# Kernel tuning notes

Measured on AMD Instinct MI355X. Metric: run time of the kernel, lower is better.

## Reference

```python
import jax, jax.numpy as jnp
import numpy as np

B, N, C, H, P = 4, 8192, 256, 4, 64  # batch, tokens(=input_size), hidden, heads, proj_size
D = C // H


def setup_inputs() -> dict:
    key = jax.random.key(0)
    ks = jax.random.split(key, 12)
    s = 1.0 / np.sqrt(C)
    inp = {
        "x": jax.random.normal(ks[0], (B, N, C), jnp.float32),
        "q": jax.random.normal(ks[1], (B, N, C), jnp.float32),
        "Wq": jax.random.normal(ks[2], (C, C), jnp.float32) * s,
        "Wk": jax.random.normal(ks[3], (C, C), jnp.float32) * s,
        "Wv_ca": jax.random.normal(ks[4], (C, C), jnp.float32) * s,
        "Wv_sa": jax.random.normal(ks[5], (C, C), jnp.float32) * s,
        "E_w": jax.random.normal(ks[6], (P, N), jnp.float32) * (1.0 / np.sqrt(N)),
        "E_b": jnp.zeros((P,), jnp.float32),
        "temp": jnp.ones((H, 1, 1), jnp.float32),
        "temp2": jnp.ones((H, 1, 1), jnp.float32),
        "Wo1": jax.random.normal(ks[7], (C // 2, C), jnp.float32) * s,
        "bo1": jnp.zeros((C // 2,), jnp.float32),
        "Wo2": jax.random.normal(ks[8], (C // 2, C), jnp.float32) * s,
        "bo2": jnp.zeros((C // 2,), jnp.float32),
    }
    return inp


def _l2norm(t):
    # F.normalize(dim=-1): x / max(||x||_2, 1e-12)
    n = jnp.sqrt(jnp.sum(t * t, axis=-1, keepdims=True))
    return t / jnp.maximum(n, 1e-12)


def reference(x, q, Wq, Wk, Wv_ca, Wv_sa, E_w, E_b, temp, temp2, Wo1, bo1, Wo2, bo2):
    b, n, c = x.shape
    h, d = H, c // H

    def split(t):  # [B,N,C] -> [B,H,d,N]
        return t.reshape(b, n, h, d).transpose(0, 2, 3, 1)

    qs = split(q @ Wq.T)
    ks = split(x @ Wk.T)
    v_ca = split(x @ Wv_ca.T)
    v_sa = split(x @ Wv_sa.T)

    # Linformer-style projections E (=F) over token dim N -> P
    k_proj = jnp.einsum('bhdn,pn->bhdp', ks, E_w) + E_b   # [B,H,d,P]
    v_proj = jnp.einsum('bhdn,pn->bhdp', v_sa, E_w) + E_b  # [B,H,d,P]

    qn = _l2norm(qs)
    kn = _l2norm(ks)

    # Channel attention: [B,H,d,d]
    attn_ca = jax.nn.softmax(jnp.einsum('bhdn,bhen->bhde', qn, kn) * temp, axis=-1)
    x_ca = jnp.einsum('bhde,bhen->bhdn', attn_ca, v_ca)
    x_ca = x_ca.transpose(0, 3, 1, 2).reshape(b, n, c)

    # Spatial (projected) attention: [B,H,N,P]
    attn_sa = jax.nn.softmax(jnp.einsum('bhdn,bhdp->bhnp', qn, k_proj) * temp2, axis=-1)
    x_sa = jnp.einsum('bhnp,bhdp->bhnd', attn_sa, v_proj)
    # faithful to original permute(0,3,1,2).reshape(B,N,C)
    x_sa = x_sa.transpose(0, 3, 1, 2).reshape(b, n, c)

    x_sa = x_sa @ Wo1.T + bo1
    x_ca = x_ca @ Wo2.T + bo2
    return jnp.concatenate((x_sa, x_ca), axis=-1)
```

## Files before the change

### kernel.cpp

```cpp
#include <hip/hip_runtime.h>
#include <hip/hip_bf16.h>

#define NN 8192
#define BNC 8388608

typedef unsigned short u16;
typedef unsigned int u32;
typedef __attribute__((ext_vector_type(8))) short bf16x8;
typedef __attribute__((ext_vector_type(4))) float f32x4;
typedef __attribute__((ext_vector_type(4))) float float4v;

__device__ __forceinline__ float bf2f(u16 u) {
    union { u32 i; float f; } c; c.i = ((u32)u) << 16; return c.f;
}
__device__ __forceinline__ u16 f2bf(float f) {
    union { float f; u32 i; } c; c.f = f;
    u32 x = c.i;
    u32 r = (x + 0x7fffu + ((x >> 16) & 1u)) >> 16;
    return (u16)r;
}
__device__ __forceinline__ void gl16(const u16* g, u16* l) {
    __builtin_amdgcn_global_load_lds(
        (const __attribute__((address_space(1))) void*)g,
        (__attribute__((address_space(3))) void*)l, 16, 0, 0);
}

__global__ void fill_kernel(float* __restrict__ out, float val) {
    int base = (blockIdx.x * 256 + threadIdx.x) * 4;
    #pragma unroll
    for (int i = 0; i < 4; ++i) out[base + i] = val;
}

__global__ void zeroconv_kernel(const float* __restrict__ x,
                                const float* __restrict__ Wq, const float* __restrict__ Wk,
                                const float* __restrict__ Wo1, const float* __restrict__ Ew,
                                u16* __restrict__ xb,
                                u16* __restrict__ Wqb, u16* __restrict__ Wkb,
                                u16* __restrict__ Wo1b, u16* __restrict__ Ewb,
                                float* __restrict__ zbase) {
    if (blockIdx.x >= 4432) {
        int i = (blockIdx.x - 4432) * 256 + threadIdx.x;
        if (i < 67584) zbase[i] = 0.f;
        return;
    }
    size_t e = ((size_t)blockIdx.x * 256 + threadIdx.x) * 8;
    const float* src; u16* dst;
    if (e < 8388608)      { src = x   + e;             dst = xb   + e; }
    else if (e < 8454144) { src = Wq  + (e - 8388608); dst = Wqb  + (e - 8388608); }
    else if (e < 8519680) { src = Wk  + (e - 8454144); dst = Wkb  + (e - 8454144); }
    else if (e < 8552448) { src = Wo1 + (e - 8519680); dst = Wo1b + (e - 8519680); }
    else                  { src = Ew  + (e - 8552448); dst = Ewb  + (e - 8552448); }
    float4v f0 = *(const float4v*)src, f1 = *(const float4v*)(src + 4);
    bf16x8 v;
    #pragma unroll
    for (int j = 0; j < 4; ++j) {
        v[j] = (short)f2bf(f0[j]); v[4 + j] = (short)f2bf(f1[j]);
    }
    *(bf16x8*)dst = v;
}

__global__ __launch_bounds__(256) void qkxe_kernel(
    const float* __restrict__ qf, const u16* __restrict__ xb,
    const u16* __restrict__ Wqb, const u16* __restrict__ Wkb,
    u16* __restrict__ Qb, u16* __restrict__ Kb,
    float* __restrict__ nq2, float* __restrict__ nk2,
    const u16* __restrict__ Ewb, float* __restrict__ xE)
{
    __shared__ u16 sm[17408];
    const int t = threadIdx.x, lane = t & 63, w = t >> 6;
    const int fr = lane & 15, fk = (lane >> 4) * 8, r0 = (lane >> 4) * 4;

    if (blockIdx.x < 1024) {
        u16* As = sm;
        u16* Bs = sm + 4096;
        const int mt = blockIdx.x & 255, nt = (blockIdx.x >> 8) & 1, z = blockIdx.x >> 9;
        const u16* Bt = z ? Wkb : Wqb;
        u16* O = z ? Kb : Qb;
        float* dstn = z ? nk2 : nq2;
        const int wr = w >> 1, wc = w & 1;
        const int m0 = mt * 128, n0 = nt * 128;
        const int b = m0 >> 13;
        const int row0 = t >> 2, k80 = (t & 3) * 8;
        const int row1 = (256 + t) >> 2, k81 = ((256 + t) & 3) * 8;

        f32x4 acc[4][4];
        #pragma unroll
        for (int i = 0; i < 4; ++i)
            #pragma unroll
            for (int j = 0; j < 4; ++j) acc[i][j] = (f32x4){0.f, 0.f, 0.f, 0.f};

        for (int kt = 0; kt < 8; ++kt) {
            const int k0 = kt * 32;
            if (z == 0) {
                const float* p0 = qf + (size_t)(m0 + row0) * 256 + k0 + k80;
                float4v f0 = *(const float4v*)p0, f1 = *(const float4v*)(p0 + 4);
                bf16x8 va;
                #pragma unroll
                for (int j = 0; j < 4; ++j) {
                    va[j] = (short)f2bf(f0[j]); va[4 + j] = (short)f2bf(f1[j]);
                }
                *(bf16x8*)&As[t * 8] = va;
                const float* p1 = qf + (size_t)(m0 + row1) * 256 + k0 + k81;
                float4v g0 = *(const float4v*)p1, g1 = *(const float4v*)(p1 + 4);
                bf16x8 vb2;
                #pragma unroll
                for (int j = 0; j < 4; ++j) {
                    vb2[j] = (short)f2bf(g0[j]); vb2[4 + j] = (short)f2bf(g1[j]);
                }
                *(bf16x8*)&As[(256 + t) * 8] = vb2;
            } else {
                gl16(xb + (size_t)(m0 + row0) * 256 + k0 + k80, &As[t * 8]);
                gl16(xb + (size_t)(m0 + row1) * 256 + k0 + k81, &As[(256 + t) * 8]);
            }
            gl16(Bt + (size_t)(n0 + row0) * 256 + k0 + k80, &Bs[t * 8]);
            gl16(Bt + (size_t)(n0 + row1) * 256 + k0 + k81, &Bs[(256 + t) * 8]);
            __syncthreads();
            bf16x8 a[4], bfr[4];
            #pragma unroll
            for (int fm = 0; fm < 4; ++fm)
                a[fm] = *(const bf16x8*)&As[(wr * 64 + fm * 16 + fr) * 32 + fk];
            #pragma unroll
            for (int fn = 0; fn < 4; ++fn)
                bfr[fn] = *(const bf16x8*)&Bs[(wc * 64 + fn * 16 + fr) * 32 + fk];
            #pragma unroll
            for (int fm = 0; fm < 4; ++fm)
                #pragma unroll
                for (int fn = 0; fn < 4; ++fn)
                    acc[fm][fn] = __builtin_amdgcn_mfma_f32_16x16x32_bf16(
                        a[fm], bfr[fn], acc[fm][fn], 0, 0, 0);
            __syncthreads();
        }

        #pragma unroll
        for (int fn = 0; fn < 4; ++fn) {
            int gcol = n0 + wc * 64 + fn * 16 + fr;
            float s = 0.f;
            #pragma unroll
            for (int fm = 0; fm < 4; ++fm) {
                #pragma unroll
                for (int r = 0; r < 4; ++r) {
                    size_t grow = (size_t)(m0 + wr * 64 + fm * 16 + r0 + r);
                    float v = acc[fm][fn][r];
                    O[grow * 256 + gcol] = f2bf(v);
                    s += v * v;
                }
            }
            s += __shfl_xor(s, 16);
            s += __shfl_xor(s, 32);
            if (lane < 16) atomicAdd(&dstn[b * 256 + gcol], s);
        }
    } else {
        u16 (*smA)[136] = (u16(*)[136])sm;
        u16 (*smB)[136] = (u16(*)[136])(sm + 8704);
        const int bx2 = blockIdx.x - 1024;
        const int bkq = bx2 >> 4, nc = bx2 & 15;
        const int b = bkq >> 2, kq = bkq & 3;

        f32x4 acc[4][4];
        #pragma unroll
        for (int i = 0; i < 4; ++i)
            #pragma unroll
            for (int j = 0; j < 4; ++j) acc[i][j] = (f32x4){0.f, 0.f, 0.f, 0.f};

        for (int it = 0; it < 4; ++it) {
            const int n0 = nc * 512 + it * 128;
            #pragma unroll
            for (int i = 0; i < 4; ++i) {
                int c = i * 256 + t, tok = c >> 3, kl = (c & 7) * 8;
                const int sw = tok ^ ((kl >> 3) << 3);
                bf16x8 v = *(const bf16x8*)(xb + ((size_t)b * NN + n0 + tok) * 256 + kq * 64 + kl);
                #pragma unroll
                for (int j = 0; j < 8; ++j) smA[kl + j][sw] = (u16)v[j];
            }
            #pragma unroll
            for (int i = 0; i < 4; ++i) {
                int c = i * 256 + t, p = c >> 4, tk8 = (c & 15) * 8;
                *(bf16x8*)&smB[p][tk8] = *(const bf16x8*)(Ewb + (size_t)p * NN + n0 + tk8);
            }
            __syncthreads();
            bf16x8 a[4], bb[4];
            #pragma unroll
            for (int fm = 0; fm < 4; ++fm) {
                int row = fm * 16 + fr;
                a[fm] = *(const bf16x8*)&smA[row][(w * 32 + fk) ^ (((row >> 3) & 7) << 3)];
            }
            #pragma unroll
            for (int fn = 0; fn < 4; ++fn)
                bb[fn] = *(const bf16x8*)&smB[fn * 16 + fr][w * 32 + fk];
            #pragma unroll
            for (int fm = 0; fm < 4; ++fm)
                #pragma unroll
                for (int fn = 0; fn < 4; ++fn)
                    acc[fm][fn] = __builtin_amdgcn_mfma_f32_16x16x32_bf16(
                        a[fm], bb[fn], acc[fm][fn], 0, 0, 0);
            __syncthreads();
        }
        float* Cred = (float*)&smA[0][0];
        for (int ph = 0; ph < 4; ++ph) {
            if (w == ph) {
                #pragma unroll
                for (int fm = 0; fm < 4; ++fm)
                    #pragma unroll
                    for (int fn = 0; fn < 4; ++fn)
                        #pragma unroll
                        for (int r = 0; r < 4; ++r) {
                            int idx = (fm * 16 + r0 + r) * 64 + fn * 16 + fr;
                            if (ph == 0) Cred[idx] = acc[fm][fn][r];
                            else         Cred[idx] += acc[fm][fn][r];
                        }
            }
            __syncthreads();
        }
        float* dst = xE + (size_t)(b * 256 + kq * 64) * 64;
        #pragma unroll
        for (int i = 0; i < 16; ++i) atomicAdd(&dst[i * 256 + t], Cred[i * 256 + t]);
    }
}

__global__ __launch_bounds__(256) void calogkv_kernel(
    const u16* __restrict__ Qb, const u16* __restrict__ Kb, float* __restrict__ cpart,
    const float* __restrict__ Wk, const float* __restrict__ Wvsa,
    const float* __restrict__ xE, const float* __restrict__ Eb,
    float* __restrict__ kp, float* __restrict__ vp)
{
    __shared__ u16 sm[17408];
    const int t = threadIdx.x, lane = t & 63, w = t >> 6;
    const int fr = lane & 15, fk = (lane >> 4) * 8, r0 = (lane >> 4) * 4;

    if (blockIdx.x < 256) {
        u16 (*smA)[136] = (u16(*)[136])sm;
        u16 (*smB)[136] = (u16(*)[136])(sm + 8704);
        const int bh = blockIdx.x >> 4, nc = blockIdx.x & 15;
        const int b = bh >> 2, h = bh & 3;

        f32x4 acc[4][4];
        #pragma unroll
        for (int i = 0; i < 4; ++i)
            #pragma unroll
            for (int j = 0; j < 4; ++j) acc[i][j] = (f32x4){0.f, 0.f, 0.f, 0.f};

        for (int it = 0; it < 4; ++it) {
            const int n0 = nc * 512 + it * 128;
            #pragma unroll
            for (int i = 0; i < 4; ++i) {
                int c = i * 256 + t, tok = c >> 3, ch8 = (c & 7) * 8;
                const int sw = tok ^ ((ch8 >> 3) << 3);
                size_t g = ((size_t)b * NN + n0 + tok) * 256 + h * 64 + ch8;
                bf16x8 vq = *(const bf16x8*)(Qb + g);
                bf16x8 vk = *(const bf16x8*)(Kb + g);
                #pragma unroll
                for (int j = 0; j < 8; ++j) {
                    smA[ch8 + j][sw] = (u16)vq[j];
                    smB[ch8 + j][sw] = (u16)vk[j];
                }
            }
            __syncthreads();
            bf16x8 a[4], bb[4];
            #pragma unroll
            for (int fm = 0; fm < 4; ++fm) {
                int row = fm * 16 + fr;
                a[fm] = *(const bf16x8*)&smA[row][(w * 32 + fk) ^ (((row >> 3) & 7) << 3)];
            }
            #pragma unroll
            for (int fn = 0; fn < 4; ++fn) {
                int row = fn * 16 + fr;
                bb[fn] = *(const bf16x8*)&smB[row][(w * 32 + fk) ^ (((row >> 3) & 7) << 3)];
            }
            #pragma unroll
            for (int fm = 0; fm < 4; ++fm)
                #pragma unroll
                for (int fn = 0; fn < 4; ++fn)
                    acc[fm][fn] = __builtin_amdgcn_mfma_f32_16x16x32_bf16(
                        a[fm], bb[fn], acc[fm][fn], 0, 0, 0);
            __syncthreads();
        }
        float* Cred = (float*)&smA[0][0];
        for (int ph = 0; ph < 4; ++ph) {
            if (w == ph) {
                #pragma unroll
                for (int fm = 0; fm < 4; ++fm)
                    #pragma unroll
                    for (int fn = 0; fn < 4; ++fn)
                        #pragma unroll
                        for (int r = 0; r < 4; ++r) {
                            int idx = (fm * 16 + r0 + r) * 64 + fn * 16 + fr;
                            if (ph == 0) Cred[idx] = acc[fm][fn][r];
                            else         Cred[idx] += acc[fm][fn][r];
                        }
            }
            __syncthreads();
        }
        float* dst = cpart + (size_t)nc * 65536 + (size_t)bh * 4096;
        #pragma unroll
        for (int i = 0; i < 16; ++i) dst[i * 256 + t] = Cred[i * 256 + t];
    } else {
        const int idx = blockIdx.x - 256;
        const int z = idx >> 8, bc4 = idx & 255;
        const int b = bc4 >> 6, c = (bc4 & 63) * 4 + (t >> 6);
        const int p = t & 63;
        const float* W = z ? Wvsa : Wk;
        float* dst = z ? vp : kp;
        float s = 0.f;
        for (int k = 0; k < 256; ++k)
            s += W[c * 256 + k] * xE[(size_t)(b * 256 + k) * 64 + p];
        dst[(size_t)(b * 256 + c) * 64 + p] = s + Eb[p];
    }
}

__global__ __launch_bounds__(256) void smsa_kernel(
    const float* __restrict__ cpart, const float* __restrict__ nq2,
    const float* __restrict__ nk2, const float* __restrict__ temp,
    float* __restrict__ caprob,
    const u16* __restrict__ Qb, const float* __restrict__ kp,
    const float* __restrict__ vp, const float* __restrict__ temp2,
    u16* __restrict__ xsa)
{
    __shared__ char smem[49152];
    const int t = threadIdx.x;
    if (blockIdx.x < 256) {
        const int row = blockIdx.x * 4 + (t >> 6);
        const int e = t & 63;
        const int b = row >> 8, c = row & 255, h = c >> 6;
        const int i = row * 64 + e;
        float lg = cpart[i];
        #pragma unroll
        for (int nc = 1; nc < 16; ++nc) lg += cpart[(size_t)nc * 65536 + i];
        float nq = fmaxf(sqrtf(nq2[row]), 1e-12f);
        float nk = fmaxf(sqrtf(nk2[b * 256 + h * 64 + e]), 1e-12f);
        float v = lg / (nq * nk) * temp[h];
        float m = v;
        #pragma unroll
        for (int o = 32; o; o >>= 1) m = fmaxf(m, __shfl_xor(m, o));
        float ex = __expf(v - m);
        float s = ex;
        #pragma unroll
        for (int o = 32; o; o >>= 1) s += __shfl_xor(s, o);
        caprob[i] = ex / s;
        return;
    }
    u16* Qs = (u16*)smem;
    u16* KT = (u16*)(smem + 32768);
    u16* VT = (u16*)(smem + 40960);
    const int bx2 = blockIdx.x - 256;
    const int nc = bx2 & 31, bh = bx2 >> 5, b = bh >> 2, h = bh & 3;
    const int lane = t & 63, w = t >> 6;
    const int fr = lane & 15, fk = (lane >> 4) * 8, r0 = (lane >> 4) * 4;

    #pragma unroll
    for (int i = 0; i < 8; ++i) {
        int c = i * 256 + t, tok = c >> 3, ch8 = (c & 7) * 8;
        *(bf16x8*)&Qs[c * 8] =
            *(const bf16x8*)(Qb + ((size_t)b * NN + nc * 256 + tok) * 256 + h * 64 + ch8);
    }
    {
        const int d = t >> 2, p0 = (t & 3) * 16;
        const float rqv = 1.0f / fmaxf(sqrtf(nq2[b * 256 + h * 64 + d]), 1e-12f);
        const float t2 = temp2[h];
        const float* kr = kp + (size_t)(b * 256 + h * 64 + d) * 64 + p0;
        #pragma unroll
        for (int j = 0; j < 16; ++j)
            KT[(p0 + j) * 64 + d] = f2bf(kr[j] * rqv * t2);
    }
    {
        const float* vs = vp + (size_t)(b * 256 + h * 64) * 64;
        #pragma unroll
        for (int i = 0; i < 2; ++i) {
            int c = i * 256 + t;
            bf16x8 v;
            #pragma unroll
            for (int j = 0; j < 8; ++j) v[j] = (short)f2bf(vs[c * 8 + j]);
            *(bf16x8*)&VT[c * 8] = v;
        }
    }
    __syncthreads();

    f32x4 acc[4][4];
    #pragma unroll
    for (int i = 0; i < 4; ++i)
        #pragma unroll
        for (int j = 0; j < 4; ++j) acc[i][j] = (f32x4){0.f, 0.f, 0.f, 0.f};
    #pragma unroll
    for (int ks = 0; ks < 2; ++ks) {
        bf16x8 a[4], bb[4];
        #pragma unroll
        for (int fm = 0; fm < 4; ++fm)
            a[fm] = *(const bf16x8*)&Qs[(w * 64 + fm * 16 + fr) * 64 + ks * 32 + fk];
        #pragma unroll
        for (int fn = 0; fn < 4; ++fn)
            bb[fn] = *(const bf16x8*)&KT[(fn * 16 + fr) * 64 + ks * 32 + fk];
        #pragma unroll
        for (int fm = 0; fm < 4; ++fm)
            #pragma unroll
            for (int fn = 0; fn < 4; ++fn)
                acc[fm][fn] = __builtin_amdgcn_mfma_f32_16x16x32_bf16(
                    a[fm], bb[fn], acc[fm][fn], 0, 0, 0);
    }
    __syncthreads();

    u16* Pw = Qs + w * 4096;
    #pragma unroll
    for (int fm = 0; fm < 4; ++fm) {
        #pragma unroll
        for (int r = 0; r < 4; ++r) {
            float m = fmaxf(fmaxf(acc[fm][0][r], acc[fm][1][r]),
                            fmaxf(acc[fm][2][r], acc[fm][3][r]));
            m = fmaxf(m, __shfl_xor(m, 1));
            m = fmaxf(m, __shfl_xor(m, 2));
            m = fmaxf(m, __shfl_xor(m, 4));
            m = fmaxf(m, __shfl_xor(m, 8));
            float e0 = __expf(acc[fm][0][r] - m), e1 = __expf(acc[fm][1][r] - m);
            float e2 = __expf(acc[fm][2][r] - m), e3 = __expf(acc[fm][3][r] - m);
            float s = e0 + e1 + e2 + e3;
            s += __shfl_xor(s, 1); s += __shfl_xor(s, 2);
            s += __shfl_xor(s, 4); s += __shfl_xor(s, 8);
            float rs = 1.0f / s;
            int row = fm * 16 + r0 + r;
            Pw[row * 64 +  0 + fr] = f2bf(e0 * rs);
            Pw[row * 64 + 16 + fr] = f2bf(e1 * rs);
            Pw[row * 64 + 32 + fr] = f2bf(e2 * rs);
            Pw[row * 64 + 48 + fr] = f2bf(e3 * rs);
        }
    }

    f32x4 acc2[4][4];
    #pragma unroll
    for (int i = 0; i < 4; ++i)
        #pragma unroll
        for (int j = 0; j < 4; ++j) acc2[i][j] = (f32x4){0.f, 0.f, 0.f, 0.f};
    #pragma unroll
    for (int ks = 0; ks < 2; ++ks) {
        bf16x8 a[4], bb[4];
        #pragma unroll
        for (int fm = 0; fm < 4; ++fm)
            a[fm] = *(const bf16x8*)&Pw[(fm * 16 + fr) * 64 + ks * 32 + fk];
        #pragma unroll
        for (int fn = 0; fn < 4; ++fn)
            bb[fn] = *(const bf16x8*)&VT[(fn * 16 + fr) * 64 + ks * 32 + fk];
        #pragma unroll
        for (int fm = 0; fm < 4; ++fm)
            #pragma unroll
            for (int fn = 0; fn < 4; ++fn)
                acc2[fm][fn] = __builtin_amdgcn_mfma_f32_16x16x32_bf16(
                    a[fm], bb[fn], acc2[fm][fn], 0, 0, 0);
    }
    __syncthreads();

    u16* X2 = Qs;
    #pragma unroll
    for (int fm = 0; fm < 4; ++fm)
        #pragma unroll
        for (int fn = 0; fn < 4; ++fn)
            #pragma unroll
            for (int r = 0; r < 4; ++r)
                X2[(w * 64 + fm * 16 + r0 + r) * 64 + fn * 16 + fr] = f2bf(acc2[fm][fn][r]);
    __syncthreads();

    {
        const int d = t >> 2, cq = (t & 3) * 64;
        u16* orow = xsa + ((size_t)b * NN + d * 128 + h * 32 + nc) * 256 + cq;
        #pragma unroll
        for (int i = 0; i < 8; ++i) {
            bf16x8 v;
            #pragma unroll
            for (int j = 0; j < 8; ++j) v[j] = (short)X2[(cq + i * 8 + j) * 64 + d];
            *(bf16x8*)&orow[i * 8] = v;
        }
    }
}

__device__ __forceinline__ void out_gemm_body(
    const u16* __restrict__ A, const u16* __restrict__ Bt,
    const float* __restrict__ bias, int outoff, int m0,
    float* __restrict__ out, u16* As, u16* Bs, int t)
{
    const int lane = t & 63, w = t >> 6;
    const int wr = w >> 1, wc = w & 1;
    const int fr = lane & 15, fk = (lane >> 4) * 8, r0 = (lane >> 4) * 4;
    const int row0 = t >> 2, k80 = (t & 3) * 8;
    const int row1 = (256 + t) >> 2, k81 = ((256 + t) & 3) * 8;

    f32x4 acc[4][4];
    #pragma unroll
    for (int i = 0; i < 4; ++i)
        #pragma unroll
        for (int j = 0; j < 4; ++j) acc[i][j] = (f32x4){0.f, 0.f, 0.f, 0.f};

    for (int kt = 0; kt < 8; ++kt) {
        const int k0 = kt * 32;
        gl16(A  + (size_t)(m0 + row0) * 256 + k0 + k80, &As[t * 8]);
        gl16(A  + (size_t)(m0 + row1) * 256 + k0 + k81, &As[(256 + t) * 8]);
        gl16(Bt + (size_t)row0 * 256 + k0 + k80, &Bs[t * 8]);
        gl16(Bt + (size_t)row1 * 256 + k0 + k81, &Bs[(256 + t) * 8]);
        __syncthreads();
        bf16x8 a[4], bfr[4];
        #pragma unroll
        for (int fm = 0; fm < 4; ++fm)
            a[fm] = *(const bf16x8*)&As[(wr * 64 + fm * 16 + fr) * 32 + fk];
        #pragma unroll
        for (int fn = 0; fn < 4; ++fn)
            bfr[fn] = *(const bf16x8*)&Bs[(wc * 64 + fn * 16 + fr) * 32 + fk];
        #pragma unroll
        for (int fm = 0; fm < 4; ++fm)
            #pragma unroll
            for (int fn = 0; fn < 4; ++fn)
                acc[fm][fn] = __builtin_amdgcn_mfma_f32_16x16x32_bf16(
                    a[fm], bfr[fn], acc[fm][fn], 0, 0, 0);
        __syncthreads();
    }

    #pragma unroll
    for (int fm = 0; fm < 4; ++fm)
        #pragma unroll
        for (int fn = 0; fn < 4; ++fn) {
            int gcol = wc * 64 + fn * 16 + fr;
            #pragma unroll
            for (int r = 0; r < 4; ++r) {
                size_t grow = (size_t)(m0 + wr * 64 + fm * 16 + r0 + r);
                out[grow * 256 + outoff + gcol] = acc[fm][fn][r] + bias[gcol];
            }
        }
}

__global__ __launch_bounds__(256) void mwout_kernel(
    const float* __restrict__ caprob, const float* __restrict__ Wo2,
    const float* __restrict__ Wvca, u16* __restrict__ W2effb,
    const u16* __restrict__ xsa, const u16* __restrict__ Wo1b,
    const float* __restrict__ bo1, float* __restrict__ out)
{
    __shared__ u16 sm[8192];
    const int t = threadIdx.x;
    if (blockIdx.x < 512) {
        float* Ml = (float*)sm;
        const int bj = blockIdx.x;
        const int b = bj >> 7, j = bj & 127;
        const int h = t >> 6, e = t & 63;
        float s = 0.f;
        #pragma unroll 8
        for (int d = 0; d < 64; ++d)
            s += Wo2[j * 256 + h * 64 + d] * caprob[(size_t)(b * 256 + h * 64 + d) * 64 + e];
        Ml[t] = s;
        __syncthreads();
        float s2 = 0.f;
        for (int c = 0; c < 256; ++c) s2 += Ml[c] * Wvca[c * 256 + t];
        W2effb[(size_t)bj * 256 + t] = f2bf(s2);
        return;
    }
    const int m0 = (blockIdx.x - 512) * 128;
    out_gemm_body(xsa, Wo1b, bo1, 0, m0, out, sm, sm + 4096, t);
}

__global__ __launch_bounds__(256) void outca_kernel(
    const u16* __restrict__ xb, const u16* __restrict__ W2effb,
    const float* __restrict__ bo2, float* __restrict__ out)
{
    __shared__ u16 sm[8192];
    const int t = threadIdx.x;
    const int m0 = blockIdx.x * 128;
    const u16* Bt = W2effb + (size_t)(blockIdx.x >> 6) * 128 * 256;
    out_gemm_body(xb, Bt, bo2, 128, m0, out, sm, sm + 4096, t);
}

extern "C" void kernel_launch(void* const* d_in, const int* in_sizes, int n_in,
                              void* d_out, int out_size, void* d_ws, size_t ws_size,
                              hipStream_t stream) {
    float* out = (float*)d_out;

    static const int expect[14] = {8388608, 8388608, 65536, 65536, 65536, 65536,
                                   524288, 64, 4, 4, 32768, 128, 32768, 128};
    bool ok = (n_in == 14) && (out_size == 8388608);
    if (ok) for (int i = 0; i < 14; ++i) ok = ok && (in_sizes[i] == expect[i]);
    if (!ok) {
        fill_kernel<<<dim3(8192), 256, 0, stream>>>(out, 3000.0f);
        return;
    }
    if (ws_size < 80000000u) {
        fill_kernel<<<dim3(8192), 256, 0, stream>>>(out, 1000.0f);
        return;
    }

    const float* x    = (const float*)d_in[0];
    const float* q    = (const float*)d_in[1];
    const float* Wq   = (const float*)d_in[2];
    const float* Wk   = (const float*)d_in[3];
    const float* Wvca = (const float*)d_in[4];
    const float* Wvsa = (const float*)d_in[5];
    const float* Ew   = (const float*)d_in[6];
    const float* Eb   = (const float*)d_in[7];
    const float* temp = (const float*)d_in[8];
    const float* temp2= (const float*)d_in[9];
    const float* Wo1  = (const float*)d_in[10];
    const float* bo1  = (const float*)d_in[11];
    const float* Wo2  = (const float*)d_in[12];
    const float* bo2  = (const float*)d_in[13];

    u16* Qb   = (u16*)d_ws;
    u16* Kb   = Qb + (size_t)BNC;
    u16* xb   = Kb + (size_t)BNC;
    u16* Wqb  = xb + (size_t)BNC;
    u16* Wkb  = Wqb + 65536;
    u16* Wo1b = Wkb + 65536;
    u16* Ewb  = Wo1b + 32768;
    u16* W2effb = Ewb + 524288;
    u16* xsa  = Kb;
    float* fs    = (float*)(W2effb + 131072);
    float* nq2   = fs;
    float* nk2   = nq2 + 1024;
    float* xE    = nk2 + 1024;
    float* kp    = xE + 65536;
    float* vp    = kp + 65536;
    float* caprob= vp + 65536;
    float* cpart = caprob + 65536;

    zeroconv_kernel<<<dim3(4696), 256, 0, stream>>>(x, Wq, Wk, Wo1, Ew,
                                                    xb, Wqb, Wkb, Wo1b, Ewb, nq2);
    qkxe_kernel<<<dim3(1280), 256, 0, stream>>>(q, xb, Wqb, Wkb, Qb, Kb, nq2, nk2,
                                                Ewb, xE);
    calogkv_kernel<<<dim3(768), 256, 0, stream>>>(Qb, Kb, cpart, Wk, Wvsa, xE, Eb, kp, vp);
    smsa_kernel<<<dim3(768), 256, 0, stream>>>(cpart, nq2, nk2, temp, caprob,
                                               Qb, kp, vp, temp2, xsa);
    mwout_kernel<<<dim3(768), 256, 0, stream>>>(caprob, Wo2, Wvca, W2effb,
                                                xsa, Wo1b, bo1, out);
    outca_kernel<<<dim3(256), 256, 0, stream>>>(xb, W2effb, bo2, out);
}
```

Before: 105.5 us.

## Use 128-wide K tiles with XOR-swizzled LDS layout in Q/K projection GEMM

The Q/K projection GEMM now stages 128-wide K chunks into LDS, so each block runs two iterations instead of eight, with four MFMA sub-steps per iteration. An XOR swizzle on the column index, applied both when loading and when reading fragments, is meant to avoid LDS bank conflicts. This cuts barrier count and load-phase overhead. In exchange, LDS use per block grows from 34 KB to 64 KB, which may reduce occupancy, and the other branches of the same kernel also carry this larger allocation.

```diff
diff --git a/kernel.cpp b/kernel.cpp
--- a/kernel.cpp
+++ b/kernel.cpp
@@ -66,13 +66,13 @@
     float* __restrict__ nq2, float* __restrict__ nk2,
     const u16* __restrict__ Ewb, float* __restrict__ xE)
 {
-    __shared__ u16 sm[17408];
+    __shared__ u16 sm[32768];
     const int t = threadIdx.x, lane = t & 63, w = t >> 6;
     const int fr = lane & 15, fk = (lane >> 4) * 8, r0 = (lane >> 4) * 4;
 
     if (blockIdx.x < 1024) {
         u16* As = sm;
-        u16* Bs = sm + 4096;
+        u16* Bs = sm + 16384;
         const int mt = blockIdx.x & 255, nt = (blockIdx.x >> 8) & 1, z = blockIdx.x >> 9;
         const u16* Bt = z ? Wkb : Wqb;
         u16* O = z ? Kb : Qb;
@@ -80,8 +80,6 @@
         const int wr = w >> 1, wc = w & 1;
         const int m0 = mt * 128, n0 = nt * 128;
         const int b = m0 >> 13;
-        const int row0 = t >> 2, k80 = (t & 3) * 8;
-        const int row1 = (256 + t) >> 2, k81 = ((256 + t) & 3) * 8;
 
         f32x4 acc[4][4];
         #pragma unroll
@@ -89,45 +87,49 @@
             #pragma unroll
             for (int j = 0; j < 4; ++j) acc[i][j] = (f32x4){0.f, 0.f, 0.f, 0.f};
 
-        for (int kt = 0; kt < 8; ++kt) {
-            const int k0 = kt * 32;
-            if (z == 0) {
-                const float* p0 = qf + (size_t)(m0 + row0) * 256 + k0 + k80;
-                float4v f0 = *(const float4v*)p0, f1 = *(const float4v*)(p0 + 4);
-                bf16x8 va;
-                #pragma unroll
-                for (int j = 0; j < 4; ++j) {
-                    va[j] = (short)f2bf(f0[j]); va[4 + j] = (short)f2bf(f1[j]);
+        for (int kt = 0; kt < 2; ++kt) {
+            const int k0 = kt * 128;
+            #pragma unroll
+            for (int i = 0; i < 8; ++i) {
+                int c = i * 256 + t, row = c >> 4, kc8 = (c & 15) * 8;
+                int ksrc = kc8 ^ ((row & 7) << 3);
+                if (z == 0) {
+                    const float* p = qf + (size_t)(m0 + row) * 256 + k0 + ksrc;
+                    float4v f0 = *(const float4v*)p, f1 = *(const float4v*)(p + 4);
+                    bf16x8 va;
+                    #pragma unroll
+                    for (int j = 0; j < 4; ++j) {
+                        va[j] = (short)f2bf(f0[j]); va[4 + j] = (short)f2bf(f1[j]);
+                    }
+                    *(bf16x8*)&As[c * 8] = va;
+                } else {
+                    gl16(xb + (size_t)(m0 + row) * 256 + k0 + ksrc, &As[c * 8]);
                 }
-                *(bf16x8*)&As[t * 8] = va;
-                const float* p1 = qf + (size_t)(m0 + row1) * 256 + k0 + k81;
-                float4v g0 = *(const float4v*)p1, g1 = *(const float4v*)(p1 + 4);
-                bf16x8 vb2;
-                #pragma unroll
-                for (int j = 0; j < 4; ++j) {
-                    vb2[j] = (short)f2bf(g0[j]); vb2[4 + j] = (short)f2bf(g1[j]);
+                gl16(Bt + (size_t)(n0 + row) * 256 + k0 + ksrc, &Bs[c * 8]);
+            }
+            __syncthreads();
+            #pragma unroll
+            for (int ks = 0; ks < 4; ++ks) {
+                bf16x8 a[4], bfr[4];
+                #pragma unroll
+                for (int fm = 0; fm < 4; ++fm) {
+                    int row = wr * 64 + fm * 16 + fr;
+                    a[fm] = *(const bf16x8*)&As[row * 128 +
+                             ((ks * 32 + fk) ^ ((row & 7) << 3))];
                 }
-                *(bf16x8*)&As[(256 + t) * 8] = vb2;
-            } else {
-                gl16(xb + (size_t)(m0 + row0) * 256 + k0 + k80, &As[t * 8]);
-                gl16(xb + (size_t)(m0 + row1) * 256 + k0 + k81, &As[(256 + t) * 8]);
-            }
-            gl16(Bt + (size_t)(n0 + row0) * 256 + k0 + k80, &Bs[t * 8]);
-            gl16(Bt + (size_t)(n0 + row1) * 256 + k0 + k81, &Bs[(256 + t) * 8]);
-            __syncthreads();
-            bf16x8 a[4], bfr[4];
-            #pragma unroll
-            for (int fm = 0; fm < 4; ++fm)
-                a[fm] = *(const bf16x8*)&As[(wr * 64 + fm * 16 + fr) * 32 + fk];
-            #pragma unroll
-            for (int fn = 0; fn < 4; ++fn)
-                bfr[fn] = *(const bf16x8*)&Bs[(wc * 64 + fn * 16 + fr) * 32 + fk];
-            #pragma unroll
-            for (int fm = 0; fm < 4; ++fm)
-                #pragma unroll
-                for (int fn = 0; fn < 4; ++fn)
-                    acc[fm][fn] = __builtin_amdgcn_mfma_f32_16x16x32_bf16(
-                        a[fm], bfr[fn], acc[fm][fn], 0, 0, 0);
+                #pragma unroll
+                for (int fn = 0; fn < 4; ++fn) {
+                    int row = wc * 64 + fn * 16 + fr;
+                    bfr[fn] = *(const bf16x8*)&Bs[row * 128 +
+                              ((ks * 32 + fk) ^ ((row & 7) << 3))];
+                }
+                #pragma unroll
+                for (int fm = 0; fm < 4; ++fm)
+                    #pragma unroll
+                    for (int fn = 0; fn < 4; ++fn)
+                        acc[fm][fn] = __builtin_amdgcn_mfma_f32_16x16x32_bf16(
+                            a[fm], bfr[fn], acc[fm][fn], 0, 0, 0);
+            }
             __syncthreads();
         }
 
```

After: 106.7 us. About the same (+1.1%).

## Move x fp32-to-bf16 conversion into qkxe kernel, consuming fp32 x directly

Applied to the files above, without the earlier changes.

The standalone conversion of x to bf16 is removed from the first kernel, which now converts only the weights and zeroes buffers. The GEMM and xE paths of qkxe read fp32 x and convert it in registers, and 4096 extra blocks in the same launch still write xb for the later kernels. This takes the full fp32-x pass off the critical path before the GEMM, so the write of xb overlaps with the compute. In exchange the GEMM reads twice as many bytes for x and loses the async LDS load path, and xb is still written in full.

```diff
diff --git a/kernel.cpp b/kernel.cpp
--- a/kernel.cpp
+++ b/kernel.cpp
@@ -31,25 +31,22 @@
     for (int i = 0; i < 4; ++i) out[base + i] = val;
 }
 
-__global__ void zeroconv_kernel(const float* __restrict__ x,
-                                const float* __restrict__ Wq, const float* __restrict__ Wk,
+__global__ void zeroconv_kernel(const float* __restrict__ Wq, const float* __restrict__ Wk,
                                 const float* __restrict__ Wo1, const float* __restrict__ Ew,
-                                u16* __restrict__ xb,
                                 u16* __restrict__ Wqb, u16* __restrict__ Wkb,
                                 u16* __restrict__ Wo1b, u16* __restrict__ Ewb,
                                 float* __restrict__ zbase) {
-    if (blockIdx.x >= 4432) {
-        int i = (blockIdx.x - 4432) * 256 + threadIdx.x;
+    if (blockIdx.x >= 336) {
+        int i = (blockIdx.x - 336) * 256 + threadIdx.x;
         if (i < 67584) zbase[i] = 0.f;
         return;
     }
     size_t e = ((size_t)blockIdx.x * 256 + threadIdx.x) * 8;
     const float* src; u16* dst;
-    if (e < 8388608)      { src = x   + e;             dst = xb   + e; }
-    else if (e < 8454144) { src = Wq  + (e - 8388608); dst = Wqb  + (e - 8388608); }
-    else if (e < 8519680) { src = Wk  + (e - 8454144); dst = Wkb  + (e - 8454144); }
-    else if (e < 8552448) { src = Wo1 + (e - 8519680); dst = Wo1b + (e - 8519680); }
-    else                  { src = Ew  + (e - 8552448); dst = Ewb  + (e - 8552448); }
+    if (e < 65536)       { src = Wq  + e;            dst = Wqb  + e; }
+    else if (e < 131072) { src = Wk  + (e - 65536);  dst = Wkb  + (e - 65536); }
+    else if (e < 163840) { src = Wo1 + (e - 131072); dst = Wo1b + (e - 131072); }
+    else                 { src = Ew  + (e - 163840); dst = Ewb  + (e - 163840); }
     float4v f0 = *(const float4v*)src, f1 = *(const float4v*)(src + 4);
     bf16x8 v;
     #pragma unroll
@@ -60,7 +57,7 @@
 }
 
 __global__ __launch_bounds__(256) void qkxe_kernel(
-    const float* __restrict__ qf, const u16* __restrict__ xb,
+    const float* __restrict__ qf, const float* __restrict__ x, u16* __restrict__ xb,
     const u16* __restrict__ Wqb, const u16* __restrict__ Wkb,
     u16* __restrict__ Qb, u16* __restrict__ Kb,
     float* __restrict__ nq2, float* __restrict__ nk2,
@@ -70,10 +67,23 @@
     const int t = threadIdx.x, lane = t & 63, w = t >> 6;
     const int fr = lane & 15, fk = (lane >> 4) * 8, r0 = (lane >> 4) * 4;
 
+    if (blockIdx.x >= 1280) {
+        size_t e = ((size_t)(blockIdx.x - 1280) * 256 + t) * 8;
+        float4v f0 = *(const float4v*)(x + e), f1 = *(const float4v*)(x + e + 4);
+        bf16x8 v;
+        #pragma unroll
+        for (int j = 0; j < 4; ++j) {
+            v[j] = (short)f2bf(f0[j]); v[4 + j] = (short)f2bf(f1[j]);
+        }
+        *(bf16x8*)(xb + e) = v;
+        return;
+    }
+
     if (blockIdx.x < 1024) {
         u16* As = sm;
         u16* Bs = sm + 4096;
         const int mt = blockIdx.x & 255, nt = (blockIdx.x >> 8) & 1, z = blockIdx.x >> 9;
+        const float* Af = z ? x : qf;
         const u16* Bt = z ? Wkb : Wqb;
         u16* O = z ? Kb : Qb;
         float* dstn = z ? nk2 : nq2;
@@ -91,8 +101,8 @@
 
         for (int kt = 0; kt < 8; ++kt) {
             const int k0 = kt * 32;
-            if (z == 0) {
-                const float* p0 = qf + (size_t)(m0 + row0) * 256 + k0 + k80;
+            {
+                const float* p0 = Af + (size_t)(m0 + row0) * 256 + k0 + k80;
                 float4v f0 = *(const float4v*)p0, f1 = *(const float4v*)(p0 + 4);
                 bf16x8 va;
                 #pragma unroll
@@ -100,7 +110,7 @@
                     va[j] = (short)f2bf(f0[j]); va[4 + j] = (short)f2bf(f1[j]);
                 }
                 *(bf16x8*)&As[t * 8] = va;
-                const float* p1 = qf + (size_t)(m0 + row1) * 256 + k0 + k81;
+                const float* p1 = Af + (size_t)(m0 + row1) * 256 + k0 + k81;
                 float4v g0 = *(const float4v*)p1, g1 = *(const float4v*)(p1 + 4);
                 bf16x8 vb2;
                 #pragma unroll
@@ -108,9 +118,6 @@
                     vb2[j] = (short)f2bf(g0[j]); vb2[4 + j] = (short)f2bf(g1[j]);
                 }
                 *(bf16x8*)&As[(256 + t) * 8] = vb2;
-            } else {
-                gl16(xb + (size_t)(m0 + row0) * 256 + k0 + k80, &As[t * 8]);
-                gl16(xb + (size_t)(m0 + row1) * 256 + k0 + k81, &As[(256 + t) * 8]);
             }
             gl16(Bt + (size_t)(n0 + row0) * 256 + k0 + k80, &Bs[t * 8]);
             gl16(Bt + (size_t)(n0 + row1) * 256 + k0 + k81, &Bs[(256 + t) * 8]);
@@ -168,9 +175,13 @@
             for (int i = 0; i < 4; ++i) {
                 int c = i * 256 + t, tok = c >> 3, kl = (c & 7) * 8;
                 const int sw = tok ^ ((kl >> 3) << 3);
-                bf16x8 v = *(const bf16x8*)(xb + ((size_t)b * NN + n0 + tok) * 256 + kq * 64 + kl);
-                #pragma unroll
-                for (int j = 0; j < 8; ++j) smA[kl + j][sw] = (u16)v[j];
+                const float* p = x + ((size_t)b * NN + n0 + tok) * 256 + kq * 64 + kl;
+                float4v f0 = *(const float4v*)p, f1 = *(const float4v*)(p + 4);
+                #pragma unroll
+                for (int j = 0; j < 4; ++j) {
+                    smA[kl + j][sw]     = f2bf(f0[j]);
+                    smA[kl + 4 + j][sw] = f2bf(f1[j]);
+                }
             }
             #pragma unroll
             for (int i = 0; i < 4; ++i) {
@@ -611,9 +622,9 @@
     float* caprob= vp + 65536;
     float* cpart = caprob + 65536;
 
-    zeroconv_kernel<<<dim3(4696), 256, 0, stream>>>(x, Wq, Wk, Wo1, Ew,
-                                                    xb, Wqb, Wkb, Wo1b, Ewb, nq2);
-    qkxe_kernel<<<dim3(1280), 256, 0, stream>>>(q, xb, Wqb, Wkb, Qb, Kb, nq2, nk2,
+    zeroconv_kernel<<<dim3(600), 256, 0, stream>>>(Wq, Wk, Wo1, Ew,
+                                                   Wqb, Wkb, Wo1b, Ewb, nq2);
+    qkxe_kernel<<<dim3(5376), 256, 0, stream>>>(q, x, xb, Wqb, Wkb, Qb, Kb, nq2, nk2,
                                                 Ewb, xE);
     calogkv_kernel<<<dim3(768), 256, 0, stream>>>(Qb, Kb, cpart, Wk, Wvsa, xE, Eb, kp, vp);
     smsa_kernel<<<dim3(768), 256, 0, stream>>>(cpart, nq2, nk2, temp, caprob,
```

Measured after the change: 112.7 us. 1.07x slower.
